# Performance work log

Measured on AMD Instinct MI355X. Metric: run time of the kernel, lower is better.

The kernel has to match this reference:

```python
import jax, jax.numpy as jnp
import numpy as np

N_NODES = 50000
N_EDGES = 800000
IN_FEAT = 128
HID = 128
OUT = 10
N_GRAPHS = 128
BN_EPS = 1e-5


def setup_inputs() -> dict:
    key = jax.random.key(0)
    ks = jax.random.split(key, 16)
    inp = {
        "n_feat": jax.random.normal(ks[0], (N_NODES, IN_FEAT), dtype=jnp.float32),
        "src": jax.random.randint(ks[1], (N_EDGES,), 0, N_NODES),
        "dst": jax.random.randint(ks[2], (N_EDGES,), 0, N_NODES),
        "graph_ids": jnp.sort(jax.random.randint(ks[3], (N_NODES,), 0, N_GRAPHS)),
        # GraphConv weights (DGL layout: weight [in, out], bias [out])
        "W1": jax.random.normal(ks[4], (IN_FEAT, HID), dtype=jnp.float32) / np.sqrt(IN_FEAT),
        "b1": jnp.zeros((HID,), dtype=jnp.float32),
        "W2": jax.random.normal(ks[5], (HID, HID), dtype=jnp.float32) / np.sqrt(HID),
        "b2": jnp.zeros((HID,), dtype=jnp.float32),
        # BatchNorm1d affine params
        "gamma": jnp.ones((HID,), dtype=jnp.float32),
        "beta": jnp.zeros((HID,), dtype=jnp.float32),
        # MLP head
        "fc1_w": jax.random.normal(ks[6], (HID, HID), dtype=jnp.float32) / np.sqrt(HID),
        "fc1_b": jnp.zeros((HID,), dtype=jnp.float32),
        "fc2_w": jax.random.normal(ks[7], (HID, OUT), dtype=jnp.float32) / np.sqrt(HID),
        "fc2_b": jnp.zeros((OUT,), dtype=jnp.float32),
    }
    return inp


def _graph_conv(x, W, b, src, dst, inv_sqrt_out, inv_sqrt_in):
    # DGL GraphConv, norm='both': h = D_in^{-1/2} A D_out^{-1/2} x W + b
    h = x * inv_sqrt_out[:, None]          # [N, d_in]
    h = h @ W                              # [N, d_out] (project before gather: fewer bytes moved)
    agg = jax.ops.segment_sum(h[src], dst, num_segments=N_NODES)  # gather + scatter-add
    return agg * inv_sqrt_in[:, None] + b


def reference(n_feat, src, dst, graph_ids, W1, b1, W2, b2, gamma, beta,
              fc1_w, fc1_b, fc2_w, fc2_b):
    ones_e = jnp.ones((N_EDGES,), dtype=jnp.float32)
    deg_out = jnp.clip(jax.ops.segment_sum(ones_e, src, num_segments=N_NODES), 1.0)
    deg_in = jnp.clip(jax.ops.segment_sum(ones_e, dst, num_segments=N_NODES), 1.0)
    inv_sqrt_out = jax.lax.rsqrt(deg_out)
    inv_sqrt_in = jax.lax.rsqrt(deg_in)

    x = jax.nn.relu(_graph_conv(n_feat, W1, b1, src, dst, inv_sqrt_out, inv_sqrt_in))
    # dropout is identity in eval mode
    x = jax.nn.relu(_graph_conv(x, W2, b2, src, dst, inv_sqrt_out, inv_sqrt_in))

    # SumPooling over graphs
    embedding = jax.ops.segment_sum(x, graph_ids, num_segments=N_GRAPHS)  # [B, HID]

    # BatchNorm1d (training-mode batch stats, biased variance like torch)
    mu = jnp.mean(embedding, axis=0)
    var = jnp.mean(jnp.square(embedding - mu), axis=0)
    h = gamma * (embedding - mu) * jax.lax.rsqrt(var + BN_EPS) + beta

    h = jax.nn.relu(h @ fc1_w + fc1_b)
    logits = h @ fc2_w + fc2_b
    return embedding, jax.nn.log_softmax(logits, axis=-1)
```

## Files before the change

### kernel.cpp

```cpp
#include <hip/hip_runtime.h>
#include <hip/hip_bf16.h>
#include <math.h>

#define N_NODES 50000
#define N_EDGES 800000
#define HID 128
#define N_GRAPHS 128
#define OUTC 10
#define BN_EPS 1e-5f

#define SCAN_B 256
#define N_SCAN_BLOCKS ((N_NODES + SCAN_B - 1) / SCAN_B)

#define POOL_CHUNK 32
#define N_POOL_BLOCKS ((N_NODES + POOL_CHUNK - 1) / POOL_CHUNK)

#define HB 80
#define HWORDS (N_NODES / 2)
#define HR_B 128
#define HR_BLOCKS ((HWORDS + HR_B - 1) / HR_B)

#define EPAD 8
#define E_SRC_CAP (N_EDGES + N_NODES * EPAD)

#define LDA 136

typedef short short8 __attribute__((ext_vector_type(8)));
typedef float floatx4 __attribute__((ext_vector_type(4)));

template <typename T, typename F>
__device__ inline T bitcast(F f) {
    union { F a; T b; } u;
    u.a = f;
    return u.b;
}

__device__ inline unsigned short f2bf(float x) {
    return __hip_bfloat16_raw(__float2bfloat16(x)).x;
}

__global__ __launch_bounds__(1024) void hist_part_kernel(const int* __restrict__ src,
                                                         const int* __restrict__ dst,
                                                         unsigned int* __restrict__ part,
                                                         const float* __restrict__ W1,
                                                         const float* __restrict__ W2,
                                                         unsigned short* __restrict__ Wp) {
    if (blockIdx.x == 2 * HB) {
        for (int q = threadIdx.x; q < 4096; q += 1024) {
            int wi = q >> 11;
            const float* __restrict__ W = wi ? W2 : W1;
            int t2 = q & 2047;
            int tile = t2 >> 6, lane = t2 & 63;
            int kc = tile >> 3, nt = tile & 7;
            int n = lane & 15, quad = lane >> 4;
            unsigned short v[8];
#pragma unroll
            for (int j = 0; j < 8; j++) {
                int k = kc * 32 + quad * 8 + j;
                v[j] = f2bf(W[k * HID + nt * 16 + n]);
            }
            *(uint4*)&Wp[(size_t)q * 8] = *(uint4*)v;
        }
        return;
    }
    __shared__ unsigned int h[HWORDS];
    for (int i = threadIdx.x; i < HWORDS; i += 1024) h[i] = 0;
    __syncthreads();
    int half = (blockIdx.x >= HB) ? 1 : 0;
    const int* __restrict__ idx = half ? dst : src;
    int b = blockIdx.x - half * HB;
    for (int e = b * 1024 + threadIdx.x; e < N_EDGES; e += HB * 1024) {
        int v = idx[e];
        atomicAdd(&h[v >> 1], 1u << ((v & 1) << 4));
    }
    __syncthreads();
    unsigned int* __restrict__ out = part + (size_t)blockIdx.x * HWORDS;
    for (int i = threadIdx.x; i < HWORDS; i += 1024) out[i] = h[i];
}

__global__ __launch_bounds__(HR_B) void hist_reduce_kernel(unsigned int* __restrict__ part,
                                                           int* __restrict__ cnt_in,
                                                           float* __restrict__ inv_out,
                                                           float* __restrict__ inv_in,
                                                           int* __restrict__ bsum) {
    int w = blockIdx.x * HR_B + threadIdx.x;
    int padsum = 0;
    if (w < HWORDS) {
        unsigned int s = 0, d = 0;
        for (int b = 0; b < HB; b++) {
            s += part[(size_t)b * HWORDS + w];
            unsigned int c = part[(size_t)(b + HB) * HWORDS + w];
            part[(size_t)(b + HB) * HWORDS + w] = d;
            d += c;
        }
        int i0 = w * 2, i1 = i0 + 1;
        int so0 = (int)(s & 0xFFFFu), so1 = (int)(s >> 16);
        int di0 = (int)(d & 0xFFFFu), di1 = (int)(d >> 16);
        cnt_in[i0] = di0;
        cnt_in[i1] = di1;
        inv_out[i0] = rsqrtf(fmaxf((float)so0, 1.0f));
        inv_out[i1] = rsqrtf(fmaxf((float)so1, 1.0f));
        inv_in[i0] = rsqrtf(fmaxf((float)di0, 1.0f));
        inv_in[i1] = rsqrtf(fmaxf((float)di1, 1.0f));
        padsum = ((di0 + EPAD - 1) & ~(EPAD - 1)) + ((di1 + EPAD - 1) & ~(EPAD - 1));
    }
    __shared__ int red[HR_B];
    red[threadIdx.x] = padsum;
    __syncthreads();
    for (int o = HR_B / 2; o > 0; o >>= 1) {
        if (threadIdx.x < o) red[threadIdx.x] += red[threadIdx.x + o];
        __syncthreads();
    }
    if (threadIdx.x == 0) bsum[blockIdx.x] = red[0];
}

__global__ void scan_write_kernel(const int* __restrict__ cnt, const int* __restrict__ bsum,
                                  int* __restrict__ row_ptr, int* __restrict__ edge_src) {
    __shared__ int sb[SCAN_B];
    __shared__ int part[SCAN_B];
    int t = threadIdx.x;
    sb[t] = (t < N_SCAN_BLOCKS) ? bsum[t] : 0;
    __syncthreads();
    for (int off = 1; off < SCAN_B; off <<= 1) {
        int u = (t >= off) ? sb[t - off] : 0;
        __syncthreads();
        sb[t] += u;
        __syncthreads();
    }
    int boff = (blockIdx.x == 0) ? 0 : sb[blockIdx.x - 1];

    int i = blockIdx.x * SCAN_B + t;
    int raw = (i < N_NODES) ? cnt[i] : 0;
    int v = (raw + EPAD - 1) & ~(EPAD - 1);
    part[t] = v;
    __syncthreads();
    for (int off = 1; off < SCAN_B; off <<= 1) {
        int u = (t >= off) ? part[t - off] : 0;
        __syncthreads();
        part[t] += u;
        __syncthreads();
    }
    if (i < N_NODES) {
        int ex = part[t] - v + boff;
        row_ptr[i] = ex;
        for (int p = ex + raw; p < ex + v; p++) edge_src[p] = N_NODES;
        if (i == N_NODES - 1) row_ptr[N_NODES] = ex + v;
    }
}

__global__ __launch_bounds__(1024) void csr_fill_kernel(const int* __restrict__ src,
                                                        const int* __restrict__ dst,
                                                        const unsigned int* __restrict__ part,
                                                        const int* __restrict__ row_ptr,
                                                        int* __restrict__ edge_src) {
    __shared__ unsigned int loc[HWORDS];
    int b = blockIdx.x;
    const unsigned int* __restrict__ off = part + (size_t)(b + HB) * HWORDS;
    for (int i = threadIdx.x; i < HWORDS; i += 1024) loc[i] = off[i];
    __syncthreads();
    for (int e = b * 1024 + threadIdx.x; e < N_EDGES; e += HB * 1024) {
        int d = dst[e];
        unsigned int old = atomicAdd(&loc[d >> 1], 1u << ((d & 1) << 4));
        int local = (d & 1) ? (int)(old >> 16) : (int)(old & 0xFFFFu);
        edge_src[row_ptr[d] + local] = src[e];
    }
}

__device__ inline void mm_tail(const unsigned short* __restrict__ xs,
                               const unsigned short* __restrict__ Wp,
                               __hip_bfloat16* __restrict__ Y, int row0) {
    int tid = threadIdx.x;
    int wave = tid >> 6, lane = tid & 63;
    int m = lane & 15, quad = lane >> 4;
    int rowl = wave * 16;

    short8 a[4];
#pragma unroll
    for (int kc = 0; kc < 4; kc++)
        a[kc] = bitcast<short8>(*(const uint4*)&xs[(rowl + m) * LDA + kc * 32 + quad * 8]);

    floatx4 acc[8];
#pragma unroll
    for (int nt = 0; nt < 8; nt++) acc[nt] = (floatx4){0.f, 0.f, 0.f, 0.f};

#pragma unroll
    for (int nt = 0; nt < 8; nt++) {
#pragma unroll
        for (int kc = 0; kc < 4; kc++) {
            short8 bfr = bitcast<short8>(
                *(const uint4*)&Wp[((size_t)(kc * 8 + nt) * 64 + lane) * 8]);
            acc[nt] = __builtin_amdgcn_mfma_f32_16x16x32_bf16(a[kc], bfr, acc[nt], 0, 0, 0);
        }
    }

#pragma unroll
    for (int nt = 0; nt < 8; nt++) {
#pragma unroll
        for (int i = 0; i < 4; i++) {
            int rg = row0 + rowl + quad * 4 + i;
            if (rg < N_NODES + 1) {
                Y[(size_t)rg * HID + nt * 16 + m] = __float2bfloat16(acc[nt][i]);
            }
        }
    }
}

__global__ __launch_bounds__(256) void matmul_kernel(const float* __restrict__ X,
                                                     const float* __restrict__ scale,
                                                     const unsigned short* __restrict__ Wp,
                                                     __hip_bfloat16* __restrict__ Y) {
    __shared__ unsigned short xs[64 * LDA];
    int tid = threadIdx.x;
    int row0 = blockIdx.x * 64;
    for (int j = 0; j < 8; j++) {
        int idx4 = j * 256 + tid;
        int r = idx4 >> 5;
        int col = (idx4 & 31) * 4;
        int rg = row0 + r;
        float4 v = make_float4(0.f, 0.f, 0.f, 0.f);
        if (rg < N_NODES) {
            v = *(const float4*)&X[(size_t)rg * HID + col];
            float sc = scale[rg];
            v.x *= sc; v.y *= sc; v.z *= sc; v.w *= sc;
        }
        unsigned short o[4];
        o[0] = f2bf(v.x); o[1] = f2bf(v.y); o[2] = f2bf(v.z); o[3] = f2bf(v.w);
        *(ushort4*)&xs[r * LDA + col] = *(ushort4*)o;
    }
    __syncthreads();
    mm_tail(xs, Wp, Y, row0);
}

__global__ __launch_bounds__(256) void matmul_bf16_kernel(const __hip_bfloat16* __restrict__ Xb,
                                                          const unsigned short* __restrict__ Wp,
                                                          __hip_bfloat16* __restrict__ Y) {
    __shared__ unsigned short xs[64 * LDA];
    int tid = threadIdx.x;
    int row0 = blockIdx.x * 64;
    for (int j = 0; j < 4; j++) {
        int idx8 = j * 256 + tid;
        int r = idx8 >> 4;
        int c = (idx8 & 15) * 8;
        int rg = row0 + r;
        uint4 v = make_uint4(0u, 0u, 0u, 0u);
        if (rg < N_NODES) v = *(const uint4*)&Xb[(size_t)rg * HID + c];
        *(uint4*)&xs[r * LDA + c] = v;
    }
    __syncthreads();
    mm_tail(xs, Wp, Y, row0);
}

template <bool BF16OUT>
__global__ __launch_bounds__(256) void agg_kernel_t(const __hip_bfloat16* __restrict__ Y,
                                                    const int* __restrict__ edge_src,
                                                    const int* __restrict__ row_ptr,
                                                    const float* __restrict__ inv_in,
                                                    const float* __restrict__ inv_out,
                                                    const float* __restrict__ bias,
                                                    void* __restrict__ Xout) {
    const uint4* __restrict__ Yq = (const uint4*)Y;
    int wave = threadIdx.x >> 6;
    int lane = threadIdx.x & 63;
    int n = blockIdx.x * 4 + wave;
    if (n >= N_NODES) return;
    int beg = row_ptr[n], end = row_ptr[n + 1];
    int esub = lane >> 4;
    int f16  = lane & 15;
    float acc[8] = {};
    for (int base = beg; base < end; base += 64) {
        int mm = min(64, end - base);
        int idx = (lane < mm) ? edge_src[base + lane] : N_NODES;
        for (int j = 0; j < mm; j += 8) {
            int s0 = __shfl(idx, j + esub);
            int s1 = __shfl(idx, j + 4 + esub);
            uint4 u0 = Yq[s0 * (HID / 8) + f16];
            uint4 u1 = Yq[s1 * (HID / 8) + f16];
            acc[0] += __uint_as_float(u0.x << 16); acc[1] += __uint_as_float(u0.x & 0xFFFF0000u);
            acc[2] += __uint_as_float(u0.y << 16); acc[3] += __uint_as_float(u0.y & 0xFFFF0000u);
            acc[4] += __uint_as_float(u0.z << 16); acc[5] += __uint_as_float(u0.z & 0xFFFF0000u);
            acc[6] += __uint_as_float(u0.w << 16); acc[7] += __uint_as_float(u0.w & 0xFFFF0000u);
            acc[0] += __uint_as_float(u1.x << 16); acc[1] += __uint_as_float(u1.x & 0xFFFF0000u);
            acc[2] += __uint_as_float(u1.y << 16); acc[3] += __uint_as_float(u1.y & 0xFFFF0000u);
            acc[4] += __uint_as_float(u1.z << 16); acc[5] += __uint_as_float(u1.z & 0xFFFF0000u);
            acc[6] += __uint_as_float(u1.w << 16); acc[7] += __uint_as_float(u1.w & 0xFFFF0000u);
        }
    }
#pragma unroll
    for (int i = 0; i < 8; i++) {
        acc[i] += __shfl_xor(acc[i], 16);
        acc[i] += __shfl_xor(acc[i], 32);
    }
    if (lane < 16) {
        float si = inv_in[n];
        int f0 = f16 * 8;
        float4 b0 = *(const float4*)&bias[f0];
        float4 b1 = *(const float4*)&bias[f0 + 4];
        float o[8];
        o[0] = fmaxf(acc[0] * si + b0.x, 0.f);
        o[1] = fmaxf(acc[1] * si + b0.y, 0.f);
        o[2] = fmaxf(acc[2] * si + b0.z, 0.f);
        o[3] = fmaxf(acc[3] * si + b0.w, 0.f);
        o[4] = fmaxf(acc[4] * si + b1.x, 0.f);
        o[5] = fmaxf(acc[5] * si + b1.y, 0.f);
        o[6] = fmaxf(acc[6] * si + b1.z, 0.f);
        o[7] = fmaxf(acc[7] * si + b1.w, 0.f);
        if constexpr (BF16OUT) {
            float so = inv_out[n];
            unsigned short u[8];
#pragma unroll
            for (int i = 0; i < 8; i++) u[i] = f2bf(o[i] * so);
            *(uint4*)&((__hip_bfloat16*)Xout)[(size_t)n * HID + f0] = *(uint4*)u;
        } else {
            float* Xf = (float*)Xout;
            *(float4*)&Xf[(size_t)n * HID + f0] = make_float4(o[0], o[1], o[2], o[3]);
            *(float4*)&Xf[(size_t)n * HID + f0 + 4] = make_float4(o[4], o[5], o[6], o[7]);
        }
    }
}

__global__ __launch_bounds__(64) void pool_kernel(const float* __restrict__ X,
                                                  const int* __restrict__ gid,
                                                  float* __restrict__ emb) {
    int lane = threadIdx.x;
    int n0 = blockIdx.x * POOL_CHUNK;
    int n1 = min(n0 + POOL_CHUNK, N_NODES);
    if (n0 >= N_NODES) return;
    int g_cur = gid[n0];
    float ax = 0.f, ay = 0.f;
    for (int n = n0; n < n1; n++) {
        int g = gid[n];
        if (g != g_cur) {
            atomicAdd(&emb[g_cur * HID + lane * 2], ax);
            atomicAdd(&emb[g_cur * HID + lane * 2 + 1], ay);
            ax = 0.f; ay = 0.f;
            g_cur = g;
        }
        float2 v = *(const float2*)&X[(size_t)n * HID + lane * 2];
        ax += v.x;
        ay += v.y;
    }
    atomicAdd(&emb[g_cur * HID + lane * 2], ax);
    atomicAdd(&emb[g_cur * HID + lane * 2 + 1], ay);
}

__global__ __launch_bounds__(128) void head_fused_kernel(const float* __restrict__ emb,
                                                         const float* __restrict__ gamma,
                                                         const float* __restrict__ beta,
                                                         const float* __restrict__ fc1_w,
                                                         const float* __restrict__ fc1_b,
                                                         const float* __restrict__ fc2_w,
                                                         const float* __restrict__ fc2_b,
                                                         float* __restrict__ out) {
    int r = blockIdx.x, f = threadIdx.x;
    float s = 0.f;
    for (int row = 0; row < N_GRAPHS; row++) s += emb[row * HID + f];
    float mu = s * (1.f / N_GRAPHS);
    float v = 0.f;
    for (int row = 0; row < N_GRAPHS; row++) {
        float d = emb[row * HID + f] - mu;
        v += d * d;
    }
    v *= (1.f / N_GRAPHS);
    float sc = gamma[f] * rsqrtf(v + BN_EPS);
    float sh = beta[f] - mu * sc;

    __shared__ float xr[HID];
    xr[f] = emb[r * HID + f] * sc + sh;
    __syncthreads();
    float acc = fc1_b[f];
    for (int k = 0; k < HID; k++) acc += xr[k] * fc1_w[k * HID + f];
    __shared__ float hr[HID];
    hr[f] = fmaxf(acc, 0.f);
    __syncthreads();

    __shared__ float logits[OUTC];
    __shared__ float mstat[2];
    if (f < OUTC) {
        float a = fc2_b[f];
        for (int k = 0; k < HID; k++) a += hr[k] * fc2_w[k * OUTC + f];
        logits[f] = a;
    }
    __syncthreads();
    if (f == 0) {
        float m = logits[0];
        for (int o = 1; o < OUTC; o++) m = fmaxf(m, logits[o]);
        float sum = 0.f;
        for (int o = 0; o < OUTC; o++) sum += expf(logits[o] - m);
        mstat[0] = m;
        mstat[1] = logf(sum);
    }
    __syncthreads();
    if (f < OUTC) out[r * OUTC + f] = logits[f] - mstat[0] - mstat[1];
}

extern "C" void kernel_launch(void* const* d_in, const int* in_sizes, int n_in,
                              void* d_out, int out_size, void* d_ws, size_t ws_size,
                              hipStream_t stream) {
    const float* n_feat = (const float*)d_in[0];
    const int*   src    = (const int*)d_in[1];
    const int*   dst    = (const int*)d_in[2];
    const int*   gid    = (const int*)d_in[3];
    const float* W1     = (const float*)d_in[4];
    const float* b1     = (const float*)d_in[5];
    const float* W2     = (const float*)d_in[6];
    const float* b2     = (const float*)d_in[7];
    const float* gamma  = (const float*)d_in[8];
    const float* beta   = (const float*)d_in[9];
    const float* fc1_w  = (const float*)d_in[10];
    const float* fc1_b  = (const float*)d_in[11];
    const float* fc2_w  = (const float*)d_in[12];
    const float* fc2_b  = (const float*)d_in[13];

    char* wsb = (char*)d_ws;
    size_t off = 0;
    auto alloc = [&](size_t bytes) -> void* {
        void* p = wsb + off;
        off += (bytes + 255) & ~(size_t)255;
        return p;
    };
    int*   cnt_in  = (int*)alloc((size_t)N_NODES * 4);
    int*   row_ptr = (int*)alloc((size_t)(N_NODES + 1) * 4);
    int*   e_src   = (int*)alloc((size_t)E_SRC_CAP * 4);
    float* inv_out = (float*)alloc((size_t)N_NODES * 4);
    float* inv_in  = (float*)alloc((size_t)N_NODES * 4);
    void*  ybuf    = alloc((size_t)2 * HB * HWORDS * 4);
    float* X       = (float*)alloc((size_t)N_NODES * HID * 4);
    __hip_bfloat16* X1b = (__hip_bfloat16*)alloc((size_t)N_NODES * HID * 2);
    unsigned short* Wp = (unsigned short*)alloc((size_t)2 * 32 * 64 * 8 * 2);
    int*   bsum    = (int*)alloc((size_t)SCAN_B * 4);

    unsigned int*   part = (unsigned int*)ybuf;
    __hip_bfloat16* Y    = (__hip_bfloat16*)ybuf;

    float* emb_out = (float*)d_out;
    float* lsm_out = emb_out + N_GRAPHS * HID;

    hipMemsetAsync(emb_out, 0, (size_t)N_GRAPHS * HID * 4, stream);

    hist_part_kernel<<<2 * HB + 1, 1024, 0, stream>>>(src, dst, part, W1, W2, Wp);
    hist_reduce_kernel<<<HR_BLOCKS, HR_B, 0, stream>>>(part, cnt_in, inv_out, inv_in, bsum);
    scan_write_kernel<<<N_SCAN_BLOCKS, SCAN_B, 0, stream>>>(cnt_in, bsum, row_ptr, e_src);
    csr_fill_kernel<<<HB, 1024, 0, stream>>>(src, dst, part, row_ptr, e_src);

    matmul_kernel<<<(N_NODES + 64) / 64, 256, 0, stream>>>(n_feat, inv_out, Wp, Y);
    agg_kernel_t<true><<<(N_NODES + 3) / 4, 256, 0, stream>>>(Y, e_src, row_ptr, inv_in,
                                                              inv_out, b1, X1b);
    matmul_bf16_kernel<<<(N_NODES + 64) / 64, 256, 0, stream>>>(X1b, Wp + (size_t)32 * 64 * 8, Y);
    agg_kernel_t<false><<<(N_NODES + 3) / 4, 256, 0, stream>>>(Y, e_src, row_ptr, inv_in,
                                                               nullptr, b2, X);

    pool_kernel<<<N_POOL_BLOCKS, 64, 0, stream>>>(X, gid, emb_out);
    head_fused_kernel<<<N_GRAPHS, HID, 0, stream>>>(emb_out, gamma, beta, fc1_w, fc1_b,
                                                    fc2_w, fc2_b, lsm_out);
}
```

Measured before the change: 256.3 us.

## Replace LDS partial histograms with global atomic degree counts and cursor-based CSR fill

Drops the per-block shared-memory packed histograms, their 160-partition global write-out and the serial reduction over partitions. Degree counting now uses global atomics directly on two count arrays, and the CSR fill claims slots with a global atomic cursor per destination node. The inverse-sqrt degree computation moves into the scan kernel. This removes a lot of partial-histogram traffic but adds contended global atomics, and the order of edges within each row now depends on atomic timing.

```diff
diff --git a/kernel.cpp b/kernel.cpp
--- a/kernel.cpp
+++ b/kernel.cpp
@@ -15,15 +15,12 @@
 #define POOL_CHUNK 32
 #define N_POOL_BLOCKS ((N_NODES + POOL_CHUNK - 1) / POOL_CHUNK)
 
-#define HB 80
-#define HWORDS (N_NODES / 2)
-#define HR_B 128
-#define HR_BLOCKS ((HWORDS + HR_B - 1) / HR_B)
-
 #define EPAD 8
 #define E_SRC_CAP (N_EDGES + N_NODES * EPAD)
 
 #define LDA 136
+
+#define DEG_BLOCKS 400
 
 typedef short short8 __attribute__((ext_vector_type(8)));
 typedef float floatx4 __attribute__((ext_vector_type(4)));
@@ -39,13 +36,14 @@
     return __hip_bfloat16_raw(__float2bfloat16(x)).x;
 }
 
-__global__ __launch_bounds__(1024) void hist_part_kernel(const int* __restrict__ src,
-                                                         const int* __restrict__ dst,
-                                                         unsigned int* __restrict__ part,
-                                                         const float* __restrict__ W1,
-                                                         const float* __restrict__ W2,
-                                                         unsigned short* __restrict__ Wp) {
-    if (blockIdx.x == 2 * HB) {
+__global__ __launch_bounds__(1024) void deg_kernel(const int* __restrict__ src,
+                                                   const int* __restrict__ dst,
+                                                   int* __restrict__ cnt_out,
+                                                   int* __restrict__ cnt_in,
+                                                   const float* __restrict__ W1,
+                                                   const float* __restrict__ W2,
+                                                   unsigned short* __restrict__ Wp) {
+    if (blockIdx.x == DEG_BLOCKS) {
         for (int q = threadIdx.x; q < 4096; q += 1024) {
             int wi = q >> 11;
             const float* __restrict__ W = wi ? W2 : W1;
@@ -63,59 +61,33 @@
         }
         return;
     }
-    __shared__ unsigned int h[HWORDS];
-    for (int i = threadIdx.x; i < HWORDS; i += 1024) h[i] = 0;
-    __syncthreads();
-    int half = (blockIdx.x >= HB) ? 1 : 0;
-    const int* __restrict__ idx = half ? dst : src;
-    int b = blockIdx.x - half * HB;
-    for (int e = b * 1024 + threadIdx.x; e < N_EDGES; e += HB * 1024) {
-        int v = idx[e];
-        atomicAdd(&h[v >> 1], 1u << ((v & 1) << 4));
-    }
-    __syncthreads();
-    unsigned int* __restrict__ out = part + (size_t)blockIdx.x * HWORDS;
-    for (int i = threadIdx.x; i < HWORDS; i += 1024) out[i] = h[i];
-}
-
-__global__ __launch_bounds__(HR_B) void hist_reduce_kernel(unsigned int* __restrict__ part,
-                                                           int* __restrict__ cnt_in,
-                                                           float* __restrict__ inv_out,
-                                                           float* __restrict__ inv_in,
-                                                           int* __restrict__ bsum) {
-    int w = blockIdx.x * HR_B + threadIdx.x;
-    int padsum = 0;
-    if (w < HWORDS) {
-        unsigned int s = 0, d = 0;
-        for (int b = 0; b < HB; b++) {
-            s += part[(size_t)b * HWORDS + w];
-            unsigned int c = part[(size_t)(b + HB) * HWORDS + w];
-            part[(size_t)(b + HB) * HWORDS + w] = d;
-            d += c;
-        }
-        int i0 = w * 2, i1 = i0 + 1;
-        int so0 = (int)(s & 0xFFFFu), so1 = (int)(s >> 16);
-        int di0 = (int)(d & 0xFFFFu), di1 = (int)(d >> 16);
-        cnt_in[i0] = di0;
-        cnt_in[i1] = di1;
-        inv_out[i0] = rsqrtf(fmaxf((float)so0, 1.0f));
-        inv_out[i1] = rsqrtf(fmaxf((float)so1, 1.0f));
-        inv_in[i0] = rsqrtf(fmaxf((float)di0, 1.0f));
-        inv_in[i1] = rsqrtf(fmaxf((float)di1, 1.0f));
-        padsum = ((di0 + EPAD - 1) & ~(EPAD - 1)) + ((di1 + EPAD - 1) & ~(EPAD - 1));
-    }
-    __shared__ int red[HR_B];
-    red[threadIdx.x] = padsum;
-    __syncthreads();
-    for (int o = HR_B / 2; o > 0; o >>= 1) {
-        if (threadIdx.x < o) red[threadIdx.x] += red[threadIdx.x + o];
+    for (int e = blockIdx.x * 1024 + threadIdx.x; e < N_EDGES; e += DEG_BLOCKS * 1024) {
+        atomicAdd(&cnt_out[src[e]], 1);
+        atomicAdd(&cnt_in[dst[e]], 1);
+    }
+}
+
+__global__ __launch_bounds__(SCAN_B) void bsum_kernel(const int* __restrict__ cnt_in,
+                                                      int* __restrict__ bsum) {
+    __shared__ int red[SCAN_B];
+    int t = threadIdx.x;
+    int i = blockIdx.x * SCAN_B + t;
+    int c = (i < N_NODES) ? cnt_in[i] : 0;
+    red[t] = (c + EPAD - 1) & ~(EPAD - 1);
+    __syncthreads();
+    for (int o = SCAN_B / 2; o > 0; o >>= 1) {
+        if (t < o) red[t] += red[t + o];
         __syncthreads();
     }
-    if (threadIdx.x == 0) bsum[blockIdx.x] = red[0];
-}
-
-__global__ void scan_write_kernel(const int* __restrict__ cnt, const int* __restrict__ bsum,
-                                  int* __restrict__ row_ptr, int* __restrict__ edge_src) {
+    if (t == 0) bsum[blockIdx.x] = red[0];
+}
+
+__global__ void scan_write_kernel(const int* __restrict__ cnt_out,
+                                  const int* __restrict__ cnt_in,
+                                  const int* __restrict__ bsum,
+                                  int* __restrict__ row_ptr, int* __restrict__ cursor,
+                                  float* __restrict__ inv_out, float* __restrict__ inv_in,
+                                  int* __restrict__ edge_src) {
     __shared__ int sb[SCAN_B];
     __shared__ int part[SCAN_B];
     int t = threadIdx.x;
@@ -130,7 +102,7 @@
     int boff = (blockIdx.x == 0) ? 0 : sb[blockIdx.x - 1];
 
     int i = blockIdx.x * SCAN_B + t;
-    int raw = (i < N_NODES) ? cnt[i] : 0;
+    int raw = (i < N_NODES) ? cnt_in[i] : 0;
     int v = (raw + EPAD - 1) & ~(EPAD - 1);
     part[t] = v;
     __syncthreads();
@@ -143,6 +115,9 @@
     if (i < N_NODES) {
         int ex = part[t] - v + boff;
         row_ptr[i] = ex;
+        cursor[i] = ex;
+        inv_in[i] = rsqrtf(fmaxf((float)raw, 1.0f));
+        inv_out[i] = rsqrtf(fmaxf((float)cnt_out[i], 1.0f));
         for (int p = ex + raw; p < ex + v; p++) edge_src[p] = N_NODES;
         if (i == N_NODES - 1) row_ptr[N_NODES] = ex + v;
     }
@@ -150,19 +125,12 @@
 
 __global__ __launch_bounds__(1024) void csr_fill_kernel(const int* __restrict__ src,
                                                         const int* __restrict__ dst,
-                                                        const unsigned int* __restrict__ part,
-                                                        const int* __restrict__ row_ptr,
+                                                        int* __restrict__ cursor,
                                                         int* __restrict__ edge_src) {
-    __shared__ unsigned int loc[HWORDS];
-    int b = blockIdx.x;
-    const unsigned int* __restrict__ off = part + (size_t)(b + HB) * HWORDS;
-    for (int i = threadIdx.x; i < HWORDS; i += 1024) loc[i] = off[i];
-    __syncthreads();
-    for (int e = b * 1024 + threadIdx.x; e < N_EDGES; e += HB * 1024) {
+    for (int e = blockIdx.x * 1024 + threadIdx.x; e < N_EDGES; e += DEG_BLOCKS * 1024) {
         int d = dst[e];
-        unsigned int old = atomicAdd(&loc[d >> 1], 1u << ((d & 1) << 4));
-        int local = (d & 1) ? (int)(old >> 16) : (int)(old & 0xFFFFu);
-        edge_src[row_ptr[d] + local] = src[e];
+        int pos = atomicAdd(&cursor[d], 1);
+        edge_src[pos] = src[e];
     }
 }
 
@@ -418,29 +386,30 @@
         off += (bytes + 255) & ~(size_t)255;
         return p;
     };
+    int*   cnt_out = (int*)alloc((size_t)N_NODES * 4);
     int*   cnt_in  = (int*)alloc((size_t)N_NODES * 4);
+    int*   cursor  = (int*)alloc((size_t)N_NODES * 4);
     int*   row_ptr = (int*)alloc((size_t)(N_NODES + 1) * 4);
     int*   e_src   = (int*)alloc((size_t)E_SRC_CAP * 4);
     float* inv_out = (float*)alloc((size_t)N_NODES * 4);
     float* inv_in  = (float*)alloc((size_t)N_NODES * 4);
-    void*  ybuf    = alloc((size_t)2 * HB * HWORDS * 4);
+    __hip_bfloat16* Y = (__hip_bfloat16*)alloc((size_t)(N_NODES + 1) * HID * 2);
     float* X       = (float*)alloc((size_t)N_NODES * HID * 4);
     __hip_bfloat16* X1b = (__hip_bfloat16*)alloc((size_t)N_NODES * HID * 2);
     unsigned short* Wp = (unsigned short*)alloc((size_t)2 * 32 * 64 * 8 * 2);
     int*   bsum    = (int*)alloc((size_t)SCAN_B * 4);
 
-    unsigned int*   part = (unsigned int*)ybuf;
-    __hip_bfloat16* Y    = (__hip_bfloat16*)ybuf;
-
     float* emb_out = (float*)d_out;
     float* lsm_out = emb_out + N_GRAPHS * HID;
 
+    hipMemsetAsync(cnt_out, 0, (size_t)2 * ((N_NODES * 4 + 255) & ~255), stream);
     hipMemsetAsync(emb_out, 0, (size_t)N_GRAPHS * HID * 4, stream);
 
-    hist_part_kernel<<<2 * HB + 1, 1024, 0, stream>>>(src, dst, part, W1, W2, Wp);
-    hist_reduce_kernel<<<HR_BLOCKS, HR_B, 0, stream>>>(part, cnt_in, inv_out, inv_in, bsum);
-    scan_write_kernel<<<N_SCAN_BLOCKS, SCAN_B, 0, stream>>>(cnt_in, bsum, row_ptr, e_src);
-    csr_fill_kernel<<<HB, 1024, 0, stream>>>(src, dst, part, row_ptr, e_src);
+    deg_kernel<<<DEG_BLOCKS + 1, 1024, 0, stream>>>(src, dst, cnt_out, cnt_in, W1, W2, Wp);
+    bsum_kernel<<<N_SCAN_BLOCKS, SCAN_B, 0, stream>>>(cnt_in, bsum);
+    scan_write_kernel<<<N_SCAN_BLOCKS, SCAN_B, 0, stream>>>(cnt_out, cnt_in, bsum, row_ptr,
+                                                            cursor, inv_out, inv_in, e_src);
+    csr_fill_kernel<<<DEG_BLOCKS, 1024, 0, stream>>>(src, dst, cursor, e_src);
 
     matmul_kernel<<<(N_NODES + 64) / 64, 256, 0, stream>>>(n_feat, inv_out, Wp, Y);
     agg_kernel_t<true><<<(N_NODES + 3) / 4, 256, 0, stream>>>(Y, e_src, row_ptr, inv_in,
```

New measurement: 331.5 us. 29.3% more time.

## Fuse scan and first matmul into one launch, unroll aggregation gather loop

Applied to the files above, without the earlier changes.

Merges the degree scan/row-pointer kernel, the first projection matmul and the embedding zeroing into a single launch, with block ranges dispatching to each role. Y now gets its own buffer instead of aliasing the histogram partials, so the matmul can run before csr_fill consumes those partials. The aggregation inner loop is unrolled to issue four gathers per iteration for more memory-level parallelism. The costs are extra workspace memory and higher register pressure in the aggregation kernel.

```diff
diff --git a/kernel.cpp b/kernel.cpp
--- a/kernel.cpp
+++ b/kernel.cpp
@@ -24,6 +24,8 @@
 #define E_SRC_CAP (N_EDGES + N_NODES * EPAD)
 
 #define LDA 136
+
+#define MM_BLOCKS ((N_NODES + 64) / 64)
 
 typedef short short8 __attribute__((ext_vector_type(8)));
 typedef float floatx4 __attribute__((ext_vector_type(4)));
@@ -114,11 +116,86 @@
     if (threadIdx.x == 0) bsum[blockIdx.x] = red[0];
 }
 
-__global__ void scan_write_kernel(const int* __restrict__ cnt, const int* __restrict__ bsum,
-                                  int* __restrict__ row_ptr, int* __restrict__ edge_src) {
-    __shared__ int sb[SCAN_B];
-    __shared__ int part[SCAN_B];
+__device__ inline void mm_tail(const unsigned short* __restrict__ xs,
+                               const unsigned short* __restrict__ Wp,
+                               __hip_bfloat16* __restrict__ Y, int row0) {
+    int tid = threadIdx.x;
+    int wave = tid >> 6, lane = tid & 63;
+    int m = lane & 15, quad = lane >> 4;
+    int rowl = wave * 16;
+
+    short8 a[4];
+#pragma unroll
+    for (int kc = 0; kc < 4; kc++)
+        a[kc] = bitcast<short8>(*(const uint4*)&xs[(rowl + m) * LDA + kc * 32 + quad * 8]);
+
+    floatx4 acc[8];
+#pragma unroll
+    for (int nt = 0; nt < 8; nt++) acc[nt] = (floatx4){0.f, 0.f, 0.f, 0.f};
+
+#pragma unroll
+    for (int nt = 0; nt < 8; nt++) {
+#pragma unroll
+        for (int kc = 0; kc < 4; kc++) {
+            short8 bfr = bitcast<short8>(
+                *(const uint4*)&Wp[((size_t)(kc * 8 + nt) * 64 + lane) * 8]);
+            acc[nt] = __builtin_amdgcn_mfma_f32_16x16x32_bf16(a[kc], bfr, acc[nt], 0, 0, 0);
+        }
+    }
+
+#pragma unroll
+    for (int nt = 0; nt < 8; nt++) {
+#pragma unroll
+        for (int i = 0; i < 4; i++) {
+            int rg = row0 + rowl + quad * 4 + i;
+            if (rg < N_NODES + 1) {
+                Y[(size_t)rg * HID + nt * 16 + m] = __float2bfloat16(acc[nt][i]);
+            }
+        }
+    }
+}
+
+__global__ __launch_bounds__(256) void scanmm1_kernel(const int* __restrict__ cnt,
+                                                      const int* __restrict__ bsum,
+                                                      int* __restrict__ row_ptr,
+                                                      int* __restrict__ edge_src,
+                                                      const float* __restrict__ X,
+                                                      const float* __restrict__ scale,
+                                                      const unsigned short* __restrict__ Wp,
+                                                      __hip_bfloat16* __restrict__ Y,
+                                                      float* __restrict__ emb) {
+    __shared__ unsigned short xs[64 * LDA];
     int t = threadIdx.x;
+    int b = blockIdx.x;
+
+    if (b >= N_SCAN_BLOCKS) {
+        if (b == N_SCAN_BLOCKS + MM_BLOCKS) {
+            for (int i = t; i < N_GRAPHS * HID; i += 256) emb[i] = 0.f;
+            return;
+        }
+        int row0 = (b - N_SCAN_BLOCKS) * 64;
+        for (int j = 0; j < 8; j++) {
+            int idx4 = j * 256 + t;
+            int r = idx4 >> 5;
+            int col = (idx4 & 31) * 4;
+            int rg = row0 + r;
+            float4 v = make_float4(0.f, 0.f, 0.f, 0.f);
+            if (rg < N_NODES) {
+                v = *(const float4*)&X[(size_t)rg * HID + col];
+                float sc = scale[rg];
+                v.x *= sc; v.y *= sc; v.z *= sc; v.w *= sc;
+            }
+            unsigned short o[4];
+            o[0] = f2bf(v.x); o[1] = f2bf(v.y); o[2] = f2bf(v.z); o[3] = f2bf(v.w);
+            *(ushort4*)&xs[r * LDA + col] = *(ushort4*)o;
+        }
+        __syncthreads();
+        mm_tail(xs, Wp, Y, row0);
+        return;
+    }
+
+    int* sb = (int*)xs;
+    int* part = (int*)xs + 256;
     sb[t] = (t < N_SCAN_BLOCKS) ? bsum[t] : 0;
     __syncthreads();
     for (int off = 1; off < SCAN_B; off <<= 1) {
@@ -127,9 +204,9 @@
         sb[t] += u;
         __syncthreads();
     }
-    int boff = (blockIdx.x == 0) ? 0 : sb[blockIdx.x - 1];
-
-    int i = blockIdx.x * SCAN_B + t;
+    int boff = (b == 0) ? 0 : sb[b - 1];
+
+    int i = b * SCAN_B + t;
     int raw = (i < N_NODES) ? cnt[i] : 0;
     int v = (raw + EPAD - 1) & ~(EPAD - 1);
     part[t] = v;
@@ -164,71 +241,6 @@
         int local = (d & 1) ? (int)(old >> 16) : (int)(old & 0xFFFFu);
         edge_src[row_ptr[d] + local] = src[e];
     }
-}
-
-__device__ inline void mm_tail(const unsigned short* __restrict__ xs,
-                               const unsigned short* __restrict__ Wp,
-                               __hip_bfloat16* __restrict__ Y, int row0) {
-    int tid = threadIdx.x;
-    int wave = tid >> 6, lane = tid & 63;
-    int m = lane & 15, quad = lane >> 4;
-    int rowl = wave * 16;
-
-    short8 a[4];
-#pragma unroll
-    for (int kc = 0; kc < 4; kc++)
-        a[kc] = bitcast<short8>(*(const uint4*)&xs[(rowl + m) * LDA + kc * 32 + quad * 8]);
-
-    floatx4 acc[8];
-#pragma unroll
-    for (int nt = 0; nt < 8; nt++) acc[nt] = (floatx4){0.f, 0.f, 0.f, 0.f};
-
-#pragma unroll
-    for (int nt = 0; nt < 8; nt++) {
-#pragma unroll
-        for (int kc = 0; kc < 4; kc++) {
-            short8 bfr = bitcast<short8>(
-                *(const uint4*)&Wp[((size_t)(kc * 8 + nt) * 64 + lane) * 8]);
-            acc[nt] = __builtin_amdgcn_mfma_f32_16x16x32_bf16(a[kc], bfr, acc[nt], 0, 0, 0);
-        }
-    }
-
-#pragma unroll
-    for (int nt = 0; nt < 8; nt++) {
-#pragma unroll
-        for (int i = 0; i < 4; i++) {
-            int rg = row0 + rowl + quad * 4 + i;
-            if (rg < N_NODES + 1) {
-                Y[(size_t)rg * HID + nt * 16 + m] = __float2bfloat16(acc[nt][i]);
-            }
-        }
-    }
-}
-
-__global__ __launch_bounds__(256) void matmul_kernel(const float* __restrict__ X,
-                                                     const float* __restrict__ scale,
-                                                     const unsigned short* __restrict__ Wp,
-                                                     __hip_bfloat16* __restrict__ Y) {
-    __shared__ unsigned short xs[64 * LDA];
-    int tid = threadIdx.x;
-    int row0 = blockIdx.x * 64;
-    for (int j = 0; j < 8; j++) {
-        int idx4 = j * 256 + tid;
-        int r = idx4 >> 5;
-        int col = (idx4 & 31) * 4;
-        int rg = row0 + r;
-        float4 v = make_float4(0.f, 0.f, 0.f, 0.f);
-        if (rg < N_NODES) {
-            v = *(const float4*)&X[(size_t)rg * HID + col];
-            float sc = scale[rg];
-            v.x *= sc; v.y *= sc; v.z *= sc; v.w *= sc;
-        }
-        unsigned short o[4];
-        o[0] = f2bf(v.x); o[1] = f2bf(v.y); o[2] = f2bf(v.z); o[3] = f2bf(v.w);
-        *(ushort4*)&xs[r * LDA + col] = *(ushort4*)o;
-    }
-    __syncthreads();
-    mm_tail(xs, Wp, Y, row0);
 }
 
 __global__ __launch_bounds__(256) void matmul_bf16_kernel(const __hip_bfloat16* __restrict__ Xb,
@@ -249,6 +261,12 @@
     __syncthreads();
     mm_tail(xs, Wp, Y, row0);
 }
+
+#define ACC8(u)                                                                              \
+    acc[0] += __uint_as_float(u.x << 16); acc[1] += __uint_as_float(u.x & 0xFFFF0000u);      \
+    acc[2] += __uint_as_float(u.y << 16); acc[3] += __uint_as_float(u.y & 0xFFFF0000u);      \
+    acc[4] += __uint_as_float(u.z << 16); acc[5] += __uint_as_float(u.z & 0xFFFF0000u);      \
+    acc[6] += __uint_as_float(u.w << 16); acc[7] += __uint_as_float(u.w & 0xFFFF0000u);
 
 template <bool BF16OUT>
 __global__ __launch_bounds__(256) void agg_kernel_t(const __hip_bfloat16* __restrict__ Y,
@@ -270,19 +288,24 @@
     for (int base = beg; base < end; base += 64) {
         int mm = min(64, end - base);
         int idx = (lane < mm) ? edge_src[base + lane] : N_NODES;
-        for (int j = 0; j < mm; j += 8) {
+        int j = 0;
+        for (; j + 16 <= mm; j += 16) {
+            int s0 = __shfl(idx, j + esub);
+            int s1 = __shfl(idx, j + 4 + esub);
+            int s2 = __shfl(idx, j + 8 + esub);
+            int s3 = __shfl(idx, j + 12 + esub);
+            uint4 u0 = Yq[s0 * (HID / 8) + f16];
+            uint4 u1 = Yq[s1 * (HID / 8) + f16];
+            uint4 u2 = Yq[s2 * (HID / 8) + f16];
+            uint4 u3 = Yq[s3 * (HID / 8) + f16];
+            ACC8(u0); ACC8(u1); ACC8(u2); ACC8(u3);
+        }
+        if (j < mm) {
             int s0 = __shfl(idx, j + esub);
             int s1 = __shfl(idx, j + 4 + esub);
             uint4 u0 = Yq[s0 * (HID / 8) + f16];
             uint4 u1 = Yq[s1 * (HID / 8) + f16];
-            acc[0] += __uint_as_float(u0.x << 16); acc[1] += __uint_as_float(u0.x & 0xFFFF0000u);
-            acc[2] += __uint_as_float(u0.y << 16); acc[3] += __uint_as_float(u0.y & 0xFFFF0000u);
-            acc[4] += __uint_as_float(u0.z << 16); acc[5] += __uint_as_float(u0.z & 0xFFFF0000u);
-            acc[6] += __uint_as_float(u0.w << 16); acc[7] += __uint_as_float(u0.w & 0xFFFF0000u);
-            acc[0] += __uint_as_float(u1.x << 16); acc[1] += __uint_as_float(u1.x & 0xFFFF0000u);
-            acc[2] += __uint_as_float(u1.y << 16); acc[3] += __uint_as_float(u1.y & 0xFFFF0000u);
-            acc[4] += __uint_as_float(u1.z << 16); acc[5] += __uint_as_float(u1.z & 0xFFFF0000u);
-            acc[6] += __uint_as_float(u1.w << 16); acc[7] += __uint_as_float(u1.w & 0xFFFF0000u);
+            ACC8(u0); ACC8(u1);
         }
     }
 #pragma unroll
@@ -423,29 +446,25 @@
     int*   e_src   = (int*)alloc((size_t)E_SRC_CAP * 4);
     float* inv_out = (float*)alloc((size_t)N_NODES * 4);
     float* inv_in  = (float*)alloc((size_t)N_NODES * 4);
-    void*  ybuf    = alloc((size_t)2 * HB * HWORDS * 4);
+    unsigned int* part = (unsigned int*)alloc((size_t)2 * HB * HWORDS * 4);
+    __hip_bfloat16* Y  = (__hip_bfloat16*)alloc((size_t)(N_NODES + 1) * HID * 2);
     float* X       = (float*)alloc((size_t)N_NODES * HID * 4);
     __hip_bfloat16* X1b = (__hip_bfloat16*)alloc((size_t)N_NODES * HID * 2);
     unsigned short* Wp = (unsigned short*)alloc((size_t)2 * 32 * 64 * 8 * 2);
     int*   bsum    = (int*)alloc((size_t)SCAN_B * 4);
 
-    unsigned int*   part = (unsigned int*)ybuf;
-    __hip_bfloat16* Y    = (__hip_bfloat16*)ybuf;
-
     float* emb_out = (float*)d_out;
     float* lsm_out = emb_out + N_GRAPHS * HID;
 
-    hipMemsetAsync(emb_out, 0, (size_t)N_GRAPHS * HID * 4, stream);
-
     hist_part_kernel<<<2 * HB + 1, 1024, 0, stream>>>(src, dst, part, W1, W2, Wp);
     hist_reduce_kernel<<<HR_BLOCKS, HR_B, 0, stream>>>(part, cnt_in, inv_out, inv_in, bsum);
-    scan_write_kernel<<<N_SCAN_BLOCKS, SCAN_B, 0, stream>>>(cnt_in, bsum, row_ptr, e_src);
+    scanmm1_kernel<<<N_SCAN_BLOCKS + MM_BLOCKS + 1, 256, 0, stream>>>(
+        cnt_in, bsum, row_ptr, e_src, n_feat, inv_out, Wp, Y, emb_out);
     csr_fill_kernel<<<HB, 1024, 0, stream>>>(src, dst, part, row_ptr, e_src);
 
-    matmul_kernel<<<(N_NODES + 64) / 64, 256, 0, stream>>>(n_feat, inv_out, Wp, Y);
     agg_kernel_t<true><<<(N_NODES + 3) / 4, 256, 0, stream>>>(Y, e_src, row_ptr, inv_in,
                                                               inv_out, b1, X1b);
-    matmul_bf16_kernel<<<(N_NODES + 64) / 64, 256, 0, stream>>>(X1b, Wp + (size_t)32 * 64 * 8, Y);
+    matmul_bf16_kernel<<<MM_BLOCKS, 256, 0, stream>>>(X1b, Wp + (size_t)32 * 64 * 8, Y);
     agg_kernel_t<false><<<(N_NODES + 3) / 4, 256, 0, stream>>>(Y, e_src, row_ptr, inv_in,
                                                                nullptr, b2, X);
 
```

Result: faster. 244.7 us (-4.5%).
